# Kernel tuning notes

Hardware: AMD Instinct MI355X
Metric: run time of the kernel (lower is better)

Reference implementation:

```python
import jax, jax.numpy as jnp
import numpy as np
from jax import lax

B, C, H, W = 4, 256, 128, 128
NH = 8
HD = C // NH  # 32
K = 7         # toodd(7) -> 7
DIL = 2
NBH = K // 2  # neighborhood radius


def _window_start(i, L, k, d):
    nh = k // 2
    if d <= 1:
        return max(i - nh, 0) + (L - i - nh - 1 if i + nh >= L else 0)
    ni = i - nh * d
    if ni < 0:
        return i % d
    if i + nh * d >= L:
        imodd = i % d
        a = (L // d) * d
        b = L - a
        if imodd < b:
            return L - b + imodd - 2 * nh * d
        return a + imodd - k * d
    return ni


def _pb_start(i, L, k, d):
    nh = k // 2
    if d <= 1:
        return nh + (nh - i if i < nh else 0) + (L - i - 1 - nh if i + nh >= L else 0)
    if i - nh * d < 0:
        return k - 1 - (i // d)
    if i + nh * d >= L:
        return (L - i - 1) // d
    return nh


# [L, K] neighbor indices per axis, and [L] relative-position-bias start offsets
IDX_H = np.array([[_window_start(i, H, K, DIL) + ki * DIL for ki in range(K)] for i in range(H)], dtype=np.int32)
IDX_W = np.array([[_window_start(j, W, K, DIL) + kj * DIL for kj in range(K)] for j in range(W)], dtype=np.int32)
PB_H = np.array([_pb_start(i, H, K, DIL) for i in range(H)], dtype=np.int32)
PB_W = np.array([_pb_start(j, W, K, DIL) for j in range(W)], dtype=np.int32)


def setup_inputs() -> dict:
    key = jax.random.key(0)
    ks = jax.random.split(key, 8)
    gain = 2.0 ** (-2.5)
    x = jax.random.normal(ks[0], (B, C, H, W), jnp.float32)
    # rotary tables in [-1, 1]
    sin = jax.random.uniform(ks[1], (H, W, HD), jnp.float32, minval=-1.0, maxval=1.0)
    cos = jax.random.uniform(ks[2], (H, W, HD), jnp.float32, minval=-1.0, maxval=1.0)
    w_qkv = jax.random.normal(ks[3], (3 * C, C), jnp.float32) * gain * (2.0 / (4 * C)) ** 0.5
    b_qkv = jnp.zeros((3 * C,), jnp.float32)
    w_lepe = jax.random.normal(ks[4], (C, 1, 5, 5), jnp.float32) * 0.02
    b_lepe = jnp.zeros((C,), jnp.float32)
    w_proj = jax.random.normal(ks[5], (C, C), jnp.float32) * gain * (1.0 / C) ** 0.5
    b_proj = jnp.zeros((C,), jnp.float32)
    rpb = jax.random.normal(ks[6], (NH, 2 * K - 1, 2 * K - 1), jnp.float32) * 0.02
    return {"x": x, "sin": sin, "cos": cos, "w_qkv": w_qkv, "b_qkv": b_qkv,
            "w_lepe": w_lepe, "b_lepe": b_lepe, "w_proj": w_proj, "b_proj": b_proj, "rpb": rpb}


def _rotate_every_two(t):
    t1 = t[..., ::2]
    t2 = t[..., 1::2]
    return jnp.stack([-t2, t1], axis=-1).reshape(t.shape)


def _forward(x, sin, cos, w_qkv, b_qkv, w_lepe, b_lepe, w_proj, b_proj, rpb):
    Bx, Cx, Hx, Wx = x.shape
    # 1x1 qkv conv
    qkv = jnp.einsum('oc,bchw->bohw', w_qkv, x) + b_qkv[None, :, None, None]
    v_chan = qkv[:, 2 * Cx:]
    # LePE: depthwise 5x5 conv on v channels
    lepe = lax.conv_general_dilated(v_chan, w_lepe, (1, 1), [(2, 2), (2, 2)],
                                    feature_group_count=Cx,
                                    dimension_numbers=('NCHW', 'OIHW', 'NCHW'))
    lepe = lepe + b_lepe[None, :, None, None]

    def split_heads(t):  # [B, n*c, H, W] -> [B, n, H, W, c]
        return t.reshape(Bx, NH, HD, Hx, Wx).transpose(0, 1, 3, 4, 2)

    q = split_heads(qkv[:, :Cx])
    k = split_heads(qkv[:, Cx:2 * Cx])
    v = split_heads(v_chan)

    q = (q * cos + _rotate_every_two(q) * sin) * (HD ** -0.5)
    k = k * cos + _rotate_every_two(k) * sin

    idx_h = jnp.asarray(IDX_H)
    idx_w = jnp.asarray(IDX_W)
    pb_h = jnp.asarray(PB_H)
    pb_w = jnp.asarray(PB_W)

    # na2d_qk: dilated neighborhood scores + relative position bias
    attn_slices = []
    for ki in range(K):
        kh = jnp.take(k, idx_h[:, ki], axis=2)          # [B,n,H,W,c]
        for kj in range(K):
            khw = jnp.take(kh, idx_w[:, kj], axis=3)    # [B,n,H,W,c]
            s = jnp.einsum('bnhwc,bnhwc->bnhw', q, khw)
            bias = rpb[:, pb_h + ki][:, :, pb_w + kj]    # [n,H,W]
            attn_slices.append(s + bias[None])
    attn = jnp.stack(attn_slices, axis=-1)               # [B,n,H,W,K*K]
    attn = jax.nn.softmax(attn, axis=-1)

    # na2d_av
    out = jnp.zeros_like(v)
    idx = 0
    for ki in range(K):
        vh = jnp.take(v, idx_h[:, ki], axis=2)
        for kj in range(K):
            vhw = jnp.take(vh, idx_w[:, kj], axis=3)
            out = out + attn[..., idx, None] * vhw
            idx += 1

    out = out.transpose(0, 1, 4, 2, 3).reshape(Bx, Cx, Hx, Wx)  # merge heads
    out = out + lepe
    return jnp.einsum('oc,bchw->bohw', w_proj, out) + b_proj[None, :, None, None]


def reference(x, sin, cos, w_qkv, b_qkv, w_lepe, b_lepe, w_proj, b_proj, rpb):
    return _forward(x, sin, cos, w_qkv, b_qkv, w_lepe, b_lepe, w_proj, b_proj, rpb)
```

## Files before the change

### kernel.cpp

```cpp
#include <hip/hip_runtime.h>
#include <cstddef>

#define HW 16384
#define WID 128

typedef __attribute__((ext_vector_type(8))) short short8;
typedef __attribute__((ext_vector_type(4))) float f32x4;

#define GLD4(g, l)                                                        \
    __builtin_amdgcn_global_load_lds(                                     \
        (const __attribute__((address_space(1))) unsigned int*)(g),       \
        (__attribute__((address_space(3))) unsigned int*)(l), 4, 0, 0)

__device__ __forceinline__ int wstart(int i) {
    if (i < 6) return i & 1;
    if (i >= 122) return 114 + (i & 1);
    return i - 6;
}
__device__ __forceinline__ int pbstart(int i) {
    if (i < 6) return 6 - (i >> 1);
    if (i >= 122) return (127 - i) >> 1;
    return 3;
}

__device__ __forceinline__ unsigned short bf16rne(float f) {
    unsigned u = __builtin_bit_cast(unsigned, f);
    u += 0x7FFFu + ((u >> 16) & 1u);
    return (unsigned short)(u >> 16);
}
__device__ __forceinline__ void bsplit(float f, unsigned short& h, unsigned short& l) {
    h = bf16rne(f);
    float hf = __builtin_bit_cast(float, ((unsigned)h) << 16);
    l = bf16rne(f - hf);
}

__global__ __launch_bounds__(256) void pack_t(const float* __restrict__ src, size_t bstr,
                                              unsigned short* __restrict__ dh,
                                              unsigned short* __restrict__ dl) {
    __shared__ float sm[32][260];
    const int p0 = blockIdx.x * 256, c32 = blockIdx.y, b = blockIdx.z;
    const float* s = src + (size_t)b * bstr + (size_t)(c32 * 32) * HW + p0;
    const int t = threadIdx.x;
    const int rr = t >> 3, f = t & 7;
#pragma unroll
    for (int u = 0; u < 8; u++) {
        float4 v = *(const float4*)(s + (size_t)rr * HW + (f + 8 * u) * 4);
        *(float4*)&sm[rr][(f + 8 * u) * 4] = v;
    }
    __syncthreads();
    size_t off = ((size_t)(b * 8 + c32) * HW + p0 + t) * 32;
#pragma unroll
    for (int w = 0; w < 4; w++) {
        short8 vh, vl;
#pragma unroll
        for (int e = 0; e < 8; e++) {
            unsigned short h, lo_;
            bsplit(sm[w * 8 + e][t], h, lo_);
            vh[e] = (short)h;
            vl[e] = (short)lo_;
        }
        *(short8*)&dh[off + w * 8] = vh;
        *(short8*)&dl[off + w * 8] = vl;
    }
}

template <bool QKV>
__global__ __launch_bounds__(256, 2) void gemm_mfma(
    const float* __restrict__ Wm, const unsigned short* __restrict__ xh,
    const unsigned short* __restrict__ xl, const float* __restrict__ bias,
    const float* __restrict__ sinp, const float* __restrict__ cosp,
    float* __restrict__ Y, int NMT, int MT) {
    __shared__ unsigned short As_h[128][40], As_l[128][40];
    __shared__ unsigned short Bs_h[128][40], Bs_l[128][40];
    const int bid = blockIdx.x;
    const int xcd = bid & 7, r = bid >> 3;
    const int mt = r % NMT;
    const int q2 = r / NMT;
    const int nt = xcd * 16 + (q2 & 15);
    const int b = q2 >> 4;
    const int t = threadIdx.x;
    const int lane = t & 63, wid = t >> 6;
    const int wm = wid >> 1, wn = wid & 1;
    const int m0 = mt * 128;

    f32x4 acc[4][4];
#pragma unroll
    for (int i = 0; i < 4; i++)
#pragma unroll
        for (int j = 0; j < 4; j++) acc[i][j] = (f32x4){0.f, 0.f, 0.f, 0.f};

    const int sr = t >> 1, sh = t & 1;
    const float* arow = Wm + (size_t)(m0 + sr) * 256 + sh * 16;
    const unsigned short* bh_b = xh + ((size_t)(b * 8) * HW + (size_t)nt * 128 + sr) * 32 + sh * 16;
    const unsigned short* bl_b = xl + ((size_t)(b * 8) * HW + (size_t)nt * 128 + sr) * 32 + sh * 16;

    for (int ks = 0; ks < 8; ks++) {
        {
            const float* ap = arow + ks * 32;
#pragma unroll
            for (int g = 0; g < 2; g++) {
                float4 f0 = *(const float4*)(ap + g * 8);
                float4 f1 = *(const float4*)(ap + g * 8 + 4);
                float ff[8] = {f0.x, f0.y, f0.z, f0.w, f1.x, f1.y, f1.z, f1.w};
                short8 vh, vl;
#pragma unroll
                for (int e = 0; e < 8; e++) {
                    unsigned short h, lo_;
                    bsplit(ff[e], h, lo_);
                    vh[e] = (short)h;
                    vl[e] = (short)lo_;
                }
                *(short8*)&As_h[sr][sh * 16 + g * 8] = vh;
                *(short8*)&As_l[sr][sh * 16 + g * 8] = vl;
            }
        }
        {
            const unsigned short* bp = bh_b + (size_t)ks * HW * 32;
            const unsigned short* lp = bl_b + (size_t)ks * HW * 32;
            *(short8*)&Bs_h[sr][sh * 16] = *(const short8*)(bp);
            *(short8*)&Bs_h[sr][sh * 16 + 8] = *(const short8*)(bp + 8);
            *(short8*)&Bs_l[sr][sh * 16] = *(const short8*)(lp);
            *(short8*)&Bs_l[sr][sh * 16 + 8] = *(const short8*)(lp + 8);
        }
        __syncthreads();
        const int k8 = (lane >> 4) * 8;
        short8 a_h[4], a_l[4];
#pragma unroll
        for (int mi = 0; mi < 4; mi++) {
            int am = wm * 64 + mi * 16 + (lane & 15);
            a_h[mi] = *(const short8*)&As_h[am][k8];
            a_l[mi] = *(const short8*)&As_l[am][k8];
        }
#pragma unroll
        for (int ni = 0; ni < 4; ni++) {
            int bn = wn * 64 + ni * 16 + (lane & 15);
            short8 b_h = *(const short8*)&Bs_h[bn][k8];
            short8 b_l = *(const short8*)&Bs_l[bn][k8];
#pragma unroll
            for (int mi = 0; mi < 4; mi++) {
                acc[mi][ni] = __builtin_amdgcn_mfma_f32_16x16x32_bf16(a_h[mi], b_h, acc[mi][ni], 0, 0, 0);
                acc[mi][ni] = __builtin_amdgcn_mfma_f32_16x16x32_bf16(a_h[mi], b_l, acc[mi][ni], 0, 0, 0);
                acc[mi][ni] = __builtin_amdgcn_mfma_f32_16x16x32_bf16(a_l[mi], b_h, acc[mi][ni], 0, 0, 0);
            }
        }
        __syncthreads();
    }

    const int col = lane & 15, rq = (lane >> 4) * 4;
    const int s = QKV ? (mt >> 1) : 3;
#pragma unroll
    for (int mi = 0; mi < 4; mi++) {
        int mrow = m0 + wm * 64 + mi * 16 + rq;
        float b0 = bias[mrow], b1 = bias[mrow + 1], b2 = bias[mrow + 2], b3 = bias[mrow + 3];
#pragma unroll
        for (int ni = 0; ni < 4; ni++) {
            int p = nt * 128 + wn * 64 + ni * 16 + col;
            float v0 = acc[mi][ni][0] + b0, v1 = acc[mi][ni][1] + b1;
            float v2 = acc[mi][ni][2] + b2, v3 = acc[mi][ni][3] + b3;
            if (QKV && s < 2) {
                int d0 = (mi & 1) * 16 + rq;
                const float* cp = cosp + (size_t)p * 32 + d0;
                const float* sp = sinp + (size_t)p * 32 + d0;
                float c0 = cp[0], c1 = cp[1], c2 = cp[2], c3 = cp[3];
                float s0 = sp[0], s1 = sp[1], s2 = sp[2], s3 = sp[3];
                float n0 = v0 * c0 - v1 * s0, n1 = v1 * c1 + v0 * s1;
                float n2 = v2 * c2 - v3 * s2, n3 = v3 * c3 + v2 * s3;
                if (s == 0) {
                    const float sc = 0.17677669529663687f;
                    n0 *= sc; n1 *= sc; n2 *= sc; n3 *= sc;
                }
                v0 = n0; v1 = n1; v2 = n2; v3 = n3;
            }
            float* yp = Y + ((size_t)b * MT + mrow) * HW + p;
            yp[0] = v0;
            yp[HW] = v1;
            yp[2 * HW] = v2;
            yp[3 * HW] = v3;
        }
    }
}

#define CW 2048
#define PBUF 4096
__global__ __launch_bounds__(256) void attn_k(const float* __restrict__ qkv,
                                              const float* __restrict__ rpb,
                                              const float* __restrict__ wl,
                                              const float* __restrict__ bl,
                                              float* __restrict__ out) {
    __shared__ float sm[2 * PBUF];
    const int t = threadIdx.x;
    const int ty = t >> 7;
    const int j = t & 127;
    const int bx = blockIdx.x;
    const int ip = ((bx & 7) << 3) | (bx >> 3);
    const int i0 = ip * 2;
    const int i = i0 + ty;
    const int n = blockIdx.y, b = blockIdx.z;
    const int r0 = wstart(i0);
    const int w64 = (t >> 6) * 64;

    const float* qb = qkv + ((size_t)b * 768 + n * 32) * HW;
    const float* kb = qb + (size_t)256 * HW;
    const float* vb = qb + (size_t)512 * HW;
    const int p = i * WID + j;
    const float* qrow = qb + i0 * WID;
    const float* krow = kb + r0 * WID;
    const float* vrow = vb + r0 * WID;

    const int hs = wstart(i), ws_ = wstart(j);
    const int ph = pbstart(i), pw = pbstart(j);

    float sc[49];
    const float* rp = rpb + n * 169;
#pragma unroll
    for (int ki = 0; ki < 7; ki++)
#pragma unroll
        for (int kj = 0; kj < 7; kj++)
            sc[ki * 7 + kj] = rp[(ph + ki) * 13 + (pw + kj)];

    const int aoff = (hs - r0) * WID + ws_;

#pragma unroll
    for (int s = 0; s < 2; s++) {
        const float* kp = krow + (size_t)s * HW;
#pragma unroll
        for (int u = 0; u < 7; u++) GLD4(kp + u * 256 + t, &sm[s * CW + u * 256 + w64]);
        GLD4(qrow + (size_t)s * HW + t, &sm[s * CW + 1792 + w64]);
    }

    for (int cp = 0; cp < 16; cp++) {
        float* bc = sm + (cp & 1) * PBUF;
        float* bnx = sm + ((cp + 1) & 1) * PBUF;
        if (cp < 15) {
#pragma unroll
            for (int s = 0; s < 2; s++) {
                const int c = 2 * (cp + 1) + s;
                const float* kp = krow + (size_t)c * HW;
#pragma unroll
                for (int u = 0; u < 7; u++) GLD4(kp + u * 256 + t, &bnx[s * CW + u * 256 + w64]);
                GLD4(qrow + (size_t)c * HW + t, &bnx[s * CW + 1792 + w64]);
            }
            asm volatile("s_waitcnt vmcnt(16)" ::: "memory");
        } else {
#pragma unroll
            for (int s = 0; s < 2; s++) {
                const float* vp = vrow + (size_t)s * HW;
#pragma unroll
                for (int u = 0; u < 7; u++) GLD4(vp + u * 256 + t, &bnx[s * CW + u * 256 + w64]);
            }
            asm volatile("s_waitcnt vmcnt(14)" ::: "memory");
        }
        __builtin_amdgcn_s_barrier();
        __builtin_amdgcn_s_setprio(1);
#pragma unroll
        for (int s = 0; s < 2; s++) {
            const float* bs = bc + s * CW;
            float qc = bs[1792 + t];
            const float* smb = bs + aoff;
#pragma unroll
            for (int ki = 0; ki < 7; ki++) {
                const float* kib = smb + ki * 256;
#pragma unroll
                for (int kj = 0; kj < 7; kj++)
                    sc[ki * 7 + kj] = fmaf(qc, kib[kj * 2], sc[ki * 7 + kj]);
            }
        }
        __builtin_amdgcn_s_setprio(0);
        __builtin_amdgcn_s_barrier();
    }

    float mx = sc[0];
#pragma unroll
    for (int u = 1; u < 49; u++) mx = fmaxf(mx, sc[u]);
    float sum = 0.0f;
#pragma unroll
    for (int u = 0; u < 49; u++) {
        sc[u] = __expf(sc[u] - mx);
        sum += sc[u];
    }
    float inv = 1.0f / sum;
#pragma unroll
    for (int u = 0; u < 49; u++) sc[u] *= inv;

    float* ob = out + ((size_t)b * 768 + n * 32) * HW + p;
    const float* wbase = wl + (size_t)(n * 32) * 25;
    const float* blb = bl + n * 32;
    for (int cp = 0; cp < 16; cp++) {
        float* bc = sm + (cp & 1) * PBUF;
        float* bnx = sm + ((cp + 1) & 1) * PBUF;
        if (cp < 15) {
#pragma unroll
            for (int s = 0; s < 2; s++) {
                const int c = 2 * (cp + 1) + s;
                const float* vp = vrow + (size_t)c * HW;
#pragma unroll
                for (int u = 0; u < 7; u++) GLD4(vp + u * 256 + t, &bnx[s * CW + u * 256 + w64]);
            }
            asm volatile("s_waitcnt vmcnt(14)" ::: "memory");
        } else {
            asm volatile("s_waitcnt vmcnt(0)" ::: "memory");
        }
        __builtin_amdgcn_s_barrier();
        __builtin_amdgcn_s_setprio(1);
#pragma unroll
        for (int s = 0; s < 2; s++) {
            const int ch = 2 * cp + s;
            const float* bs = bc + s * CW;
            const float* smb = bs + aoff;
            float oc = 0.0f;
#pragma unroll
            for (int ki = 0; ki < 7; ki++) {
                const float* kib = smb + ki * 256;
#pragma unroll
                for (int kj = 0; kj < 7; kj++)
                    oc = fmaf(sc[ki * 7 + kj], kib[kj * 2], oc);
            }
            const float* wrow = wbase + ch * 25;
            float lac = blb[ch];
#pragma unroll
            for (int di = 0; di < 5; di++) {
                int ii = i + di - 2;
                if ((unsigned)ii < 128u) {
                    const float* srow = bs + (ii - r0) * WID;
                    const float* wr = wrow + di * 5;
#pragma unroll
                    for (int dj = 0; dj < 5; dj++) {
                        int jj = j + dj - 2;
                        if ((unsigned)jj < 128u)
                            lac = fmaf(wr[dj], srow[jj], lac);
                    }
                }
            }
            ob[(size_t)ch * HW] = oc + lac;
        }
        __builtin_amdgcn_s_setprio(0);
        __builtin_amdgcn_s_barrier();
    }
}

extern "C" void kernel_launch(void* const* d_in, const int* in_sizes, int n_in,
                              void* d_out, int out_size, void* d_ws, size_t ws_size,
                              hipStream_t stream) {
    const float* x = (const float*)d_in[0];
    const float* sinp = (const float*)d_in[1];
    const float* cosp = (const float*)d_in[2];
    const float* w_qkv = (const float*)d_in[3];
    const float* b_qkv = (const float*)d_in[4];
    const float* w_lepe = (const float*)d_in[5];
    const float* b_lepe = (const float*)d_in[6];
    const float* w_proj = (const float*)d_in[7];
    const float* b_proj = (const float*)d_in[8];
    const float* rpb = (const float*)d_in[9];
    float* out = (float*)d_out;

    unsigned short* xph = (unsigned short*)d_ws;
    unsigned short* xpl = xph + 16777216ull;
    float* qkvb = (float*)(xph + 33554432ull);

    pack_t<<<dim3(64, 8, 4), 256, 0, stream>>>(x, (size_t)256 * HW, xph, xpl);
    gemm_mfma<true><<<dim3(3072), 256, 0, stream>>>(w_qkv, xph, xpl, b_qkv, sinp, cosp,
                                                    qkvb, 6, 768);
    attn_k<<<dim3(64, 8, 4), 256, 0, stream>>>(qkvb, rpb, w_lepe, b_lepe, qkvb);
    pack_t<<<dim3(64, 8, 4), 256, 0, stream>>>(qkvb, (size_t)768 * HW, xph, xpl);
    gemm_mfma<false><<<dim3(1024), 256, 0, stream>>>(w_proj, xph, xpl, b_proj, nullptr, nullptr,
                                                     out, 2, 256);
}
```

Measured before the change: 406.7 us.

## Fuse bf16 split packing into attention kernel and compute four rows per block

The attention kernel now writes its output directly as packed hi/lo bf16 pairs in the layout the projection GEMM expects, which removes the separate pack_t launch and the fp32 round trip through qkvb. Each block also covers four output rows instead of two, with each thread handling rows i and i+2. The shared K/V window is 8 rows and is reused for both rows, so global loads per output drop. The cost is two 49-entry score arrays per thread, which raises register pressure (launch bounds set to 3 blocks per SM), plus a slightly larger LDS buffer.

```diff
diff --git a/kernel.cpp b/kernel.cpp
--- a/kernel.cpp
+++ b/kernel.cpp
@@ -3,6 +3,8 @@
 
 #define HW 16384
 #define WID 128
+#define CSL 2560
+#define PB 5120
 
 typedef __attribute__((ext_vector_type(8))) short short8;
 typedef __attribute__((ext_vector_type(4))) float f32x4;
@@ -180,160 +182,232 @@
     }
 }
 
-#define CW 2048
-#define PBUF 4096
-__global__ __launch_bounds__(256) void attn_k(const float* __restrict__ qkv,
-                                              const float* __restrict__ rpb,
-                                              const float* __restrict__ wl,
-                                              const float* __restrict__ bl,
-                                              float* __restrict__ out) {
-    __shared__ float sm[2 * PBUF];
+template <int O>
+__device__ __forceinline__ void qk_phase(const float* bc, int abase, int qrd,
+                                         float (&sl)[49], float (&sh)[49]) {
+#pragma unroll
+    for (int s = 0; s < 2; s++) {
+        const float* win = bc + s * CSL;
+        const float ql = win[2048 + qrd];
+        const float qh = win[2048 + qrd + 256];
+        const float* rw = win + abase;
+#pragma unroll
+        for (int u = 0; u < 7 + O; u++) {
+            float tp[7];
+#pragma unroll
+            for (int kj = 0; kj < 7; kj++) tp[kj] = rw[kj * 2];
+            if (u < 7) {
+#pragma unroll
+                for (int kj = 0; kj < 7; kj++)
+                    sl[u * 7 + kj] = fmaf(ql, tp[kj], sl[u * 7 + kj]);
+            }
+            if (u >= O) {
+#pragma unroll
+                for (int kj = 0; kj < 7; kj++)
+                    sh[(u - O) * 7 + kj] = fmaf(qh, tp[kj], sh[(u - O) * 7 + kj]);
+            }
+            rw += 2 * WID;
+        }
+    }
+}
+
+template <int O>
+__device__ __forceinline__ void pv_phase(const float* bc, int abase, int i, int j, int r0,
+                                         const float (&sl)[49], const float (&sh)[49],
+                                         const float* wlb, const float* blb, int ch0,
+                                         float (&o)[2][2]) {
+#pragma unroll
+    for (int s = 0; s < 2; s++) {
+        const float* win = bc + s * CSL;
+        float olo = 0.f, ohi = 0.f;
+        const float* rw = win + abase;
+#pragma unroll
+        for (int u = 0; u < 7 + O; u++) {
+            float tp[7];
+#pragma unroll
+            for (int kj = 0; kj < 7; kj++) tp[kj] = rw[kj * 2];
+            if (u < 7) {
+#pragma unroll
+                for (int kj = 0; kj < 7; kj++) olo = fmaf(sl[u * 7 + kj], tp[kj], olo);
+            }
+            if (u >= O) {
+#pragma unroll
+                for (int kj = 0; kj < 7; kj++) ohi = fmaf(sh[(u - O) * 7 + kj], tp[kj], ohi);
+            }
+            rw += 2 * WID;
+        }
+        const float* w = wlb + (ch0 + s) * 25;
+        float llo = blb[ch0 + s], lhi = llo;
+        const float* wb = win + (i - 2 - r0) * WID + (j - 2);
+#pragma unroll
+        for (int dd = 0; dd < 7; dd++) {
+            int ii = i - 2 + dd;
+            if ((unsigned)ii < 128u) {
+                const float* srow = wb + dd * WID;
+#pragma unroll
+                for (int dj = 0; dj < 5; dj++) {
+                    int jj = j - 2 + dj;
+                    if ((unsigned)jj < 128u) {
+                        float tv = srow[dj];
+                        if (dd <= 4) llo = fmaf(w[dd * 5 + dj], tv, llo);
+                        if (dd >= 2) lhi = fmaf(w[(dd - 2) * 5 + dj], tv, lhi);
+                    }
+                }
+            }
+        }
+        o[s][0] = olo + llo;
+        o[s][1] = ohi + lhi;
+    }
+}
+
+__global__ __launch_bounds__(256, 3) void attn_k(const float* __restrict__ qkv,
+                                                 const float* __restrict__ rpb,
+                                                 const float* __restrict__ wl,
+                                                 const float* __restrict__ bl,
+                                                 unsigned short* __restrict__ oh,
+                                                 unsigned short* __restrict__ ol) {
+    __shared__ float sm[2 * PB];
     const int t = threadIdx.x;
     const int ty = t >> 7;
     const int j = t & 127;
     const int bx = blockIdx.x;
-    const int ip = ((bx & 7) << 3) | (bx >> 3);
-    const int i0 = ip * 2;
+    const int it = ((bx & 7) << 2) | (bx >> 3);
+    const int n = blockIdx.y, b = blockIdx.z;
+    const int i0 = it * 4;
     const int i = i0 + ty;
-    const int n = blockIdx.y, b = blockIdx.z;
     const int r0 = wstart(i0);
     const int w64 = (t >> 6) * 64;
+    const int thi = t >> 7, jc = t & 127;
 
     const float* qb = qkv + ((size_t)b * 768 + n * 32) * HW;
     const float* kb = qb + (size_t)256 * HW;
     const float* vb = qb + (size_t)512 * HW;
-    const int p = i * WID + j;
-    const float* qrow = qb + i0 * WID;
-    const float* krow = kb + r0 * WID;
-    const float* vrow = vb + r0 * WID;
+
+    int woff[8];
+#pragma unroll
+    for (int u = 0; u < 8; u++) {
+        int row = r0 + 2 * u + thi;
+        if (row > 127) row = 127;
+        woff[u] = row * WID + jc;
+    }
+    const int qoff0 = (i0 + thi) * WID + jc;
+    const int qoff1 = (i0 + 2 + thi) * WID + jc;
 
     const int hs = wstart(i), ws_ = wstart(j);
-    const int ph = pbstart(i), pw = pbstart(j);
-
-    float sc[49];
-    const float* rp = rpb + n * 169;
-#pragma unroll
-    for (int ki = 0; ki < 7; ki++)
-#pragma unroll
-        for (int kj = 0; kj < 7; kj++)
-            sc[ki * 7 + kj] = rp[(ph + ki) * 13 + (pw + kj)];
-
-    const int aoff = (hs - r0) * WID + ws_;
+    const int O1 = (wstart(i + 2) - hs) >> 1;
+    const int abase = (hs - r0) * WID + ws_;
+    const int qrd = ty * 128 + j;
+
+    float sl[49], sh[49];
+    {
+        const float* rp = rpb + n * 169;
+        const int pl = pbstart(i), phh = pbstart(i + 2), pw = pbstart(j);
+#pragma unroll
+        for (int ki = 0; ki < 7; ki++)
+#pragma unroll
+            for (int kj = 0; kj < 7; kj++) {
+                sl[ki * 7 + kj] = rp[(pl + ki) * 13 + (pw + kj)];
+                sh[ki * 7 + kj] = rp[(phh + ki) * 13 + (pw + kj)];
+            }
+    }
 
 #pragma unroll
     for (int s = 0; s < 2; s++) {
-        const float* kp = krow + (size_t)s * HW;
-#pragma unroll
-        for (int u = 0; u < 7; u++) GLD4(kp + u * 256 + t, &sm[s * CW + u * 256 + w64]);
-        GLD4(qrow + (size_t)s * HW + t, &sm[s * CW + 1792 + w64]);
+        const float* kp = kb + (size_t)s * HW;
+        const float* qp = qb + (size_t)s * HW;
+#pragma unroll
+        for (int u = 0; u < 8; u++) GLD4(kp + woff[u], &sm[s * CSL + u * 256 + w64]);
+        GLD4(qp + qoff0, &sm[s * CSL + 2048 + w64]);
+        GLD4(qp + qoff1, &sm[s * CSL + 2304 + w64]);
     }
 
     for (int cp = 0; cp < 16; cp++) {
-        float* bc = sm + (cp & 1) * PBUF;
-        float* bnx = sm + ((cp + 1) & 1) * PBUF;
+        float* bc = sm + (cp & 1) * PB;
+        float* bx2 = sm + ((cp + 1) & 1) * PB;
         if (cp < 15) {
 #pragma unroll
             for (int s = 0; s < 2; s++) {
                 const int c = 2 * (cp + 1) + s;
-                const float* kp = krow + (size_t)c * HW;
-#pragma unroll
-                for (int u = 0; u < 7; u++) GLD4(kp + u * 256 + t, &bnx[s * CW + u * 256 + w64]);
-                GLD4(qrow + (size_t)c * HW + t, &bnx[s * CW + 1792 + w64]);
+                const float* kp = kb + (size_t)c * HW;
+                const float* qp = qb + (size_t)c * HW;
+#pragma unroll
+                for (int u = 0; u < 8; u++) GLD4(kp + woff[u], &bx2[s * CSL + u * 256 + w64]);
+                GLD4(qp + qoff0, &bx2[s * CSL + 2048 + w64]);
+                GLD4(qp + qoff1, &bx2[s * CSL + 2304 + w64]);
+            }
+            asm volatile("s_waitcnt vmcnt(20)" ::: "memory");
+        } else {
+#pragma unroll
+            for (int s = 0; s < 2; s++) {
+                const float* vp = vb + (size_t)s * HW;
+#pragma unroll
+                for (int u = 0; u < 8; u++) GLD4(vp + woff[u], &bx2[s * CSL + u * 256 + w64]);
+            }
+            asm volatile("s_waitcnt vmcnt(16)" ::: "memory");
+        }
+        __builtin_amdgcn_s_barrier();
+        __builtin_amdgcn_s_setprio(1);
+        if (O1) qk_phase<1>(bc, abase, qrd, sl, sh);
+        else    qk_phase<0>(bc, abase, qrd, sl, sh);
+        __builtin_amdgcn_s_setprio(0);
+        __builtin_amdgcn_s_barrier();
+    }
+
+    float mx0 = sl[0], mx1 = sh[0];
+#pragma unroll
+    for (int u = 1; u < 49; u++) {
+        mx0 = fmaxf(mx0, sl[u]);
+        mx1 = fmaxf(mx1, sh[u]);
+    }
+    float s0 = 0.f, s1 = 0.f;
+#pragma unroll
+    for (int u = 0; u < 49; u++) {
+        sl[u] = __expf(sl[u] - mx0); s0 += sl[u];
+        sh[u] = __expf(sh[u] - mx1); s1 += sh[u];
+    }
+    float inv0 = 1.f / s0, inv1 = 1.f / s1;
+#pragma unroll
+    for (int u = 0; u < 49; u++) {
+        sl[u] *= inv0;
+        sh[u] *= inv1;
+    }
+
+    const float* wlb = wl + (size_t)(n * 32) * 25;
+    const float* blb = bl + n * 32;
+    const size_t obase = ((size_t)(b * 8 + n) * HW + (size_t)i * WID + j) * 32;
+    for (int cp = 0; cp < 16; cp++) {
+        float* bc = sm + (cp & 1) * PB;
+        float* bx2 = sm + ((cp + 1) & 1) * PB;
+        if (cp < 15) {
+#pragma unroll
+            for (int s = 0; s < 2; s++) {
+                const int c = 2 * (cp + 1) + s;
+                const float* vp = vb + (size_t)c * HW;
+#pragma unroll
+                for (int u = 0; u < 8; u++) GLD4(vp + woff[u], &bx2[s * CSL + u * 256 + w64]);
             }
             asm volatile("s_waitcnt vmcnt(16)" ::: "memory");
         } else {
-#pragma unroll
-            for (int s = 0; s < 2; s++) {
-                const float* vp = vrow + (size_t)s * HW;
-#pragma unroll
-                for (int u = 0; u < 7; u++) GLD4(vp + u * 256 + t, &bnx[s * CW + u * 256 + w64]);
-            }
-            asm volatile("s_waitcnt vmcnt(14)" ::: "memory");
+            asm volatile("s_waitcnt vmcnt(0)" ::: "memory");
         }
         __builtin_amdgcn_s_barrier();
         __builtin_amdgcn_s_setprio(1);
-#pragma unroll
-        for (int s = 0; s < 2; s++) {
-            const float* bs = bc + s * CW;
-            float qc = bs[1792 + t];
-            const float* smb = bs + aoff;
-#pragma unroll
-            for (int ki = 0; ki < 7; ki++) {
-                const float* kib = smb + ki * 256;
-#pragma unroll
-                for (int kj = 0; kj < 7; kj++)
-                    sc[ki * 7 + kj] = fmaf(qc, kib[kj * 2], sc[ki * 7 + kj]);
-            }
-        }
+        float o[2][2];
+        if (O1) pv_phase<1>(bc, abase, i, j, r0, sl, sh, wlb, blb, 2 * cp, o);
+        else    pv_phase<0>(bc, abase, i, j, r0, sl, sh, wlb, blb, 2 * cp, o);
         __builtin_amdgcn_s_setprio(0);
-        __builtin_amdgcn_s_barrier();
-    }
-
-    float mx = sc[0];
-#pragma unroll
-    for (int u = 1; u < 49; u++) mx = fmaxf(mx, sc[u]);
-    float sum = 0.0f;
-#pragma unroll
-    for (int u = 0; u < 49; u++) {
-        sc[u] = __expf(sc[u] - mx);
-        sum += sc[u];
-    }
-    float inv = 1.0f / sum;
-#pragma unroll
-    for (int u = 0; u < 49; u++) sc[u] *= inv;
-
-    float* ob = out + ((size_t)b * 768 + n * 32) * HW + p;
-    const float* wbase = wl + (size_t)(n * 32) * 25;
-    const float* blb = bl + n * 32;
-    for (int cp = 0; cp < 16; cp++) {
-        float* bc = sm + (cp & 1) * PBUF;
-        float* bnx = sm + ((cp + 1) & 1) * PBUF;
-        if (cp < 15) {
-#pragma unroll
-            for (int s = 0; s < 2; s++) {
-                const int c = 2 * (cp + 1) + s;
-                const float* vp = vrow + (size_t)c * HW;
-#pragma unroll
-                for (int u = 0; u < 7; u++) GLD4(vp + u * 256 + t, &bnx[s * CW + u * 256 + w64]);
-            }
-            asm volatile("s_waitcnt vmcnt(14)" ::: "memory");
-        } else {
-            asm volatile("s_waitcnt vmcnt(0)" ::: "memory");
-        }
-        __builtin_amdgcn_s_barrier();
-        __builtin_amdgcn_s_setprio(1);
-#pragma unroll
-        for (int s = 0; s < 2; s++) {
-            const int ch = 2 * cp + s;
-            const float* bs = bc + s * CW;
-            const float* smb = bs + aoff;
-            float oc = 0.0f;
-#pragma unroll
-            for (int ki = 0; ki < 7; ki++) {
-                const float* kib = smb + ki * 256;
-#pragma unroll
-                for (int kj = 0; kj < 7; kj++)
-                    oc = fmaf(sc[ki * 7 + kj], kib[kj * 2], oc);
-            }
-            const float* wrow = wbase + ch * 25;
-            float lac = blb[ch];
-#pragma unroll
-            for (int di = 0; di < 5; di++) {
-                int ii = i + di - 2;
-                if ((unsigned)ii < 128u) {
-                    const float* srow = bs + (ii - r0) * WID;
-                    const float* wr = wrow + di * 5;
-#pragma unroll
-                    for (int dj = 0; dj < 5; dj++) {
-                        int jj = j + dj - 2;
-                        if ((unsigned)jj < 128u)
-                            lac = fmaf(wr[dj], srow[jj], lac);
-                    }
-                }
-            }
-            ob[(size_t)ch * HW] = oc + lac;
-        }
-        __builtin_amdgcn_s_setprio(0);
+        {
+            unsigned short h0, l0, h1, l1;
+            size_t ob = obase + 2 * cp;
+            bsplit(o[0][0], h0, l0);
+            bsplit(o[1][0], h1, l1);
+            *(unsigned*)&oh[ob] = (unsigned)h0 | ((unsigned)h1 << 16);
+            *(unsigned*)&ol[ob] = (unsigned)l0 | ((unsigned)l1 << 16);
+            bsplit(o[0][1], h0, l0);
+            bsplit(o[1][1], h1, l1);
+            *(unsigned*)&oh[ob + 8192] = (unsigned)h0 | ((unsigned)h1 << 16);
+            *(unsigned*)&ol[ob + 8192] = (unsigned)l0 | ((unsigned)l1 << 16);
+        }
         __builtin_amdgcn_s_barrier();
     }
 }
@@ -360,8 +434,7 @@
     pack_t<<<dim3(64, 8, 4), 256, 0, stream>>>(x, (size_t)256 * HW, xph, xpl);
     gemm_mfma<true><<<dim3(3072), 256, 0, stream>>>(w_qkv, xph, xpl, b_qkv, sinp, cosp,
                                                     qkvb, 6, 768);
-    attn_k<<<dim3(64, 8, 4), 256, 0, stream>>>(qkvb, rpb, w_lepe, b_lepe, qkvb);
-    pack_t<<<dim3(64, 8, 4), 256, 0, stream>>>(qkvb, (size_t)768 * HW, xph, xpl);
+    attn_k<<<dim3(32, 8, 4), 256, 0, stream>>>(qkvb, rpb, w_lepe, b_lepe, xph, xpl);
     gemm_mfma<false><<<dim3(1024), 256, 0, stream>>>(w_proj, xph, xpl, b_proj, nullptr, nullptr,
                                                      out, 2, 256);
 }
```

Result: slower. 964.8 us (+137.2%).
